# Kernel optimization log

Measured on AMD Instinct MI355X. Metric: run time of the kernel, lower is better.

The kernel has to match this reference:

```python
import jax, jax.numpy as jnp
from jax import lax
import numpy as np

B, T, H = 4096, 512, 32


def _rnn_layer(xs, h0, Wih, Whh, bih, bhh):
    # xs: [T, B, in], h0: [B, H]. torch RNN tanh: h_t = tanh(x W_ih^T + b_ih + h W_hh^T + b_hh)
    def step(h, x_t):
        h = jnp.tanh(x_t @ Wih.T + bih + h @ Whh.T + bhh)
        return h, h
    h_last, ys = lax.scan(step, h0, xs)
    return ys, h_last  # ys: [T, B, H]


def setup_inputs() -> dict:
    key = jax.random.key(0)
    ks = jax.random.split(key, 12)
    s = 0.1  # keep tanh out of saturation
    return {
        "x": jax.random.normal(ks[0], (B, T, 1), jnp.float32),
        "h_state": jnp.zeros((2, B, H), jnp.float32),
        "Wih0": jax.random.normal(ks[1], (H, 1), jnp.float32) * s,
        "Whh0": jax.random.normal(ks[2], (H, H), jnp.float32) * s,
        "bih0": jax.random.normal(ks[3], (H,), jnp.float32) * s,
        "bhh0": jax.random.normal(ks[4], (H,), jnp.float32) * s,
        "Wih1": jax.random.normal(ks[5], (H, H), jnp.float32) * s,
        "Whh1": jax.random.normal(ks[6], (H, H), jnp.float32) * s,
        "bih1": jax.random.normal(ks[7], (H,), jnp.float32) * s,
        "bhh1": jax.random.normal(ks[8], (H,), jnp.float32) * s,
        "Wfc": jax.random.normal(ks[9], (1, H), jnp.float32) * s,
        "bfc": jax.random.normal(ks[10], (1,), jnp.float32) * s,
    }


def reference(x, h_state, Wih0, Whh0, bih0, bhh0, Wih1, Whh1, bih1, bhh1, Wfc, bfc):
    xs = jnp.transpose(x, (1, 0, 2))  # time-major [T, B, 1]
    ys0, h0_last = _rnn_layer(xs, h_state[0], Wih0, Whh0, bih0, bhh0)
    ys1, h1_last = _rnn_layer(ys0, h_state[1], Wih1, Whh1, bih1, bhh1)
    last = ys1[-1]                      # [B, H] == r_out[:, -1, :]
    pred = (last @ Wfc.T + bfc)[:, 0]   # Linear(32,1) then squeeze(-1) -> [B]
    h_new = jnp.stack([h0_last, h1_last], axis=0)  # [2, B, H]
    return pred, h_new
```

## Files before the change

### kernel.cpp

```cpp
#include <hip/hip_runtime.h>
#include <hip/hip_bf16.h>

#define BB 4096
#define TT 512
#define HH 32

typedef __attribute__((ext_vector_type(8))) short short8;
typedef __attribute__((ext_vector_type(4))) float f32x4;

#define MFMA16 __builtin_amdgcn_mfma_f32_16x16x32_bf16
#define EXP2F  __builtin_amdgcn_exp2f

union frag_u { short8 s8; __hip_bfloat162 b2[4]; };

__global__ __launch_bounds__(64) void rnn2_mfma(
    const float* __restrict__ x,
    const float* __restrict__ hstate,
    const float* __restrict__ Wih0,
    const float* __restrict__ Whh0,
    const float* __restrict__ bih0,
    const float* __restrict__ bhh0,
    const float* __restrict__ Wih1,
    const float* __restrict__ Whh1,
    const float* __restrict__ bih1,
    const float* __restrict__ bhh1,
    const float* __restrict__ Wfc,
    const float* __restrict__ bfc,
    float* __restrict__ out)
{
    const int l = threadIdx.x;
    const int q = l >> 4;
    const int n = l & 15;
    const int b = blockIdx.x * 16 + n;

    const float SC = 2.8853900817779268f;

    const int r0 = 8 * (n >> 2) + (n & 3);
    short8 A0[2], A1i[2], A1h[2];
#pragma unroll
    for (int t = 0; t < 2; ++t) {
        const int row = r0 + 4 * t;
        const float* p0 = Whh0 + row * HH + q * 8;
        const float* p1 = Wih1 + row * HH + q * 8;
        const float* p2 = Whh1 + row * HH + q * 8;
        frag_u f0, f1, f2;
#pragma unroll
        for (int jj = 0; jj < 4; ++jj) {
            f0.b2[jj] = __float22bfloat162_rn(float2{SC * p0[2 * jj], SC * p0[2 * jj + 1]});
            f1.b2[jj] = __float22bfloat162_rn(float2{SC * p1[2 * jj], SC * p1[2 * jj + 1]});
            f2.b2[jj] = __float22bfloat162_rn(float2{SC * p2[2 * jj], SC * p2[2 * jj + 1]});
        }
        A0[t] = f0.s8; A1i[t] = f1.s8; A1h[t] = f2.s8;
    }

    float wxs[8], b0s[8], b1s[8], wfc8[8];
#pragma unroll
    for (int j = 0; j < 8; ++j) {
        const int hh = 8 * q + j;
        wxs[j]  = SC * Wih0[hh];
        b0s[j]  = SC * (bih0[hh] + bhh0[hh]);
        b1s[j]  = SC * (bih1[hh] + bhh1[hh]);
        wfc8[j] = Wfc[hh];
    }
    f32x4 c1t0, c1t1;
#pragma unroll
    for (int r = 0; r < 4; ++r) { c1t0[r] = b1s[r]; c1t1[r] = b1s[4 + r]; }

    frag_u h0f, h1f;
    {
        const float* p0 = hstate + b * HH + 8 * q;
        const float* p1 = hstate + BB * HH + b * HH + 8 * q;
#pragma unroll
        for (int jj = 0; jj < 4; ++jj) {
            h0f.b2[jj] = __float22bfloat162_rn(float2{p0[2 * jj], p0[2 * jj + 1]});
            h1f.b2[jj] = __float22bfloat162_rn(float2{p1[2 * jj], p1[2 * jj + 1]});
        }
    }
    short8 hb0 = h0f.s8, hb1 = h1f.s8;

    float hf0[8], hf1[8];

    const float4* xp = (const float4*)(x + (size_t)b * TT);
    float4 xv = xp[0];

    for (int t4 = 0; t4 < TT / 4; ++t4) {
        float4 xn = xp[(t4 < TT / 4 - 1) ? t4 + 1 : t4];
#pragma unroll
        for (int jj = 0; jj < 4; ++jj) {
            const float xt = (jj == 0) ? xv.x : (jj == 1) ? xv.y : (jj == 2) ? xv.z : xv.w;

            f32x4 db0 = MFMA16(A1h[0], hb1, c1t0, 0, 0, 0);
            f32x4 db1 = MFMA16(A1h[1], hb1, c1t1, 0, 0, 0);

            f32x4 c00, c01;
#pragma unroll
            for (int r = 0; r < 4; ++r) {
                c00[r] = fmaf(wxs[r], xt, b0s[r]);
                c01[r] = fmaf(wxs[4 + r], xt, b0s[4 + r]);
            }
            f32x4 d00 = MFMA16(A0[0], hb0, c00, 0, 0, 0);
            f32x4 d01 = MFMA16(A0[1], hb0, c01, 0, 0, 0);

            frag_u nh0;
#pragma unroll
            for (int r = 0; r < 4; ++r) {
                float e0 = EXP2F(d00[r]);
                float e1 = EXP2F(d01[r]);
                hf0[r]     = fmaf(-2.0f, __builtin_amdgcn_rcpf(e0 + 1.0f), 1.0f);
                hf0[4 + r] = fmaf(-2.0f, __builtin_amdgcn_rcpf(e1 + 1.0f), 1.0f);
            }
#pragma unroll
            for (int p2 = 0; p2 < 4; ++p2)
                nh0.b2[p2] = __float22bfloat162_rn(float2{hf0[2 * p2], hf0[2 * p2 + 1]});
            hb0 = nh0.s8;

            f32x4 d10 = MFMA16(A1i[0], hb0, db0, 0, 0, 0);
            f32x4 d11 = MFMA16(A1i[1], hb0, db1, 0, 0, 0);

            frag_u nh1;
#pragma unroll
            for (int r = 0; r < 4; ++r) {
                float e0 = EXP2F(d10[r]);
                float e1 = EXP2F(d11[r]);
                hf1[r]     = fmaf(-2.0f, __builtin_amdgcn_rcpf(e0 + 1.0f), 1.0f);
                hf1[4 + r] = fmaf(-2.0f, __builtin_amdgcn_rcpf(e1 + 1.0f), 1.0f);
            }
#pragma unroll
            for (int p2 = 0; p2 < 4; ++p2)
                nh1.b2[p2] = __float22bfloat162_rn(float2{hf1[2 * p2], hf1[2 * p2 + 1]});
            hb1 = nh1.s8;
        }
        xv = xn;
    }

    float p = 0.f;
#pragma unroll
    for (int j = 0; j < 8; ++j) p = fmaf(wfc8[j], hf1[j], p);
    p += __shfl_xor(p, 16);
    p += __shfl_xor(p, 32);
    if (q == 0) out[b] = p + bfc[0];

#pragma unroll
    for (int j = 0; j < 8; ++j) {
        out[BB + b * HH + 8 * q + j]           = hf0[j];
        out[BB + BB * HH + b * HH + 8 * q + j] = hf1[j];
    }
}

extern "C" void kernel_launch(void* const* d_in, const int* in_sizes, int n_in,
                              void* d_out, int out_size, void* d_ws, size_t ws_size,
                              hipStream_t stream) {
    const float* x      = (const float*)d_in[0];
    const float* hstate = (const float*)d_in[1];
    const float* Wih0   = (const float*)d_in[2];
    const float* Whh0   = (const float*)d_in[3];
    const float* bih0   = (const float*)d_in[4];
    const float* bhh0   = (const float*)d_in[5];
    const float* Wih1   = (const float*)d_in[6];
    const float* Whh1   = (const float*)d_in[7];
    const float* bih1   = (const float*)d_in[8];
    const float* bhh1   = (const float*)d_in[9];
    const float* Wfc    = (const float*)d_in[10];
    const float* bfc    = (const float*)d_in[11];
    float* out = (float*)d_out;

    dim3 grid(BB / 16);
    dim3 block(64);
    hipLaunchKernelGGL(rnn2_mfma, grid, block, 0, stream,
                       x, hstate, Wih0, Whh0, bih0, bhh0,
                       Wih1, Whh1, bih1, bhh1, Wfc, bfc, out);
}
```

Baseline: 223.7 us.

## Skew layer-1 and layer-0 recurrences so their MFMAs and tanh work interleave

Restructures the time loop so that layer 1 at step t and layer 0 at step t+1 run in the same iteration, with a prologue and epilogue. Each iteration issues the layer-1 input MFMAs and the next layer-0 MFMAs together, then interleaves both tanh chains. The aim is to break the serial dependency of the original order, where layer 1 waited on the freshly computed layer-0 state, and so hide MFMA and transcendental latency in this single-wave-per-block kernel. It adds code size and register pressure, and the indexing of x in the prologue and epilogue has to stay correct.

```diff
diff --git a/kernel.cpp b/kernel.cpp
--- a/kernel.cpp
+++ b/kernel.cpp
@@ -79,58 +79,103 @@
     short8 hb0 = h0f.s8, hb1 = h1f.s8;
 
     float hf0[8], hf1[8];
+    f32x4 dbp0, dbp1;
 
     const float4* xp = (const float4*)(x + (size_t)b * TT);
-    float4 xv = xp[0];
-
-    for (int t4 = 0; t4 < TT / 4; ++t4) {
-        float4 xn = xp[(t4 < TT / 4 - 1) ? t4 + 1 : t4];
-#pragma unroll
-        for (int jj = 0; jj < 4; ++jj) {
-            const float xt = (jj == 0) ? xv.x : (jj == 1) ? xv.y : (jj == 2) ? xv.z : xv.w;
-
-            f32x4 db0 = MFMA16(A1h[0], hb1, c1t0, 0, 0, 0);
-            f32x4 db1 = MFMA16(A1h[1], hb1, c1t1, 0, 0, 0);
-
-            f32x4 c00, c01;
-#pragma unroll
-            for (int r = 0; r < 4; ++r) {
-                c00[r] = fmaf(wxs[r], xt, b0s[r]);
-                c01[r] = fmaf(wxs[4 + r], xt, b0s[4 + r]);
-            }
-            f32x4 d00 = MFMA16(A0[0], hb0, c00, 0, 0, 0);
-            f32x4 d01 = MFMA16(A0[1], hb0, c01, 0, 0, 0);
-
-            frag_u nh0;
-#pragma unroll
-            for (int r = 0; r < 4; ++r) {
-                float e0 = EXP2F(d00[r]);
-                float e1 = EXP2F(d01[r]);
-                hf0[r]     = fmaf(-2.0f, __builtin_amdgcn_rcpf(e0 + 1.0f), 1.0f);
-                hf0[4 + r] = fmaf(-2.0f, __builtin_amdgcn_rcpf(e1 + 1.0f), 1.0f);
-            }
-#pragma unroll
-            for (int p2 = 0; p2 < 4; ++p2)
-                nh0.b2[p2] = __float22bfloat162_rn(float2{hf0[2 * p2], hf0[2 * p2 + 1]});
-            hb0 = nh0.s8;
-
-            f32x4 d10 = MFMA16(A1i[0], hb0, db0, 0, 0, 0);
-            f32x4 d11 = MFMA16(A1i[1], hb0, db1, 0, 0, 0);
-
-            frag_u nh1;
-#pragma unroll
-            for (int r = 0; r < 4; ++r) {
-                float e0 = EXP2F(d10[r]);
-                float e1 = EXP2F(d11[r]);
-                hf1[r]     = fmaf(-2.0f, __builtin_amdgcn_rcpf(e0 + 1.0f), 1.0f);
-                hf1[4 + r] = fmaf(-2.0f, __builtin_amdgcn_rcpf(e1 + 1.0f), 1.0f);
-            }
-#pragma unroll
-            for (int p2 = 0; p2 < 4; ++p2)
-                nh1.b2[p2] = __float22bfloat162_rn(float2{hf1[2 * p2], hf1[2 * p2 + 1]});
-            hb1 = nh1.s8;
-        }
-        xv = xn;
+    float4 xc = xp[0];
+
+    {
+        f32x4 c00, c01;
+#pragma unroll
+        for (int r = 0; r < 4; ++r) {
+            c00[r] = fmaf(wxs[r], xc.x, b0s[r]);
+            c01[r] = fmaf(wxs[4 + r], xc.x, b0s[4 + r]);
+        }
+        f32x4 d00 = MFMA16(A0[0], hb0, c00, 0, 0, 0);
+        f32x4 d01 = MFMA16(A0[1], hb0, c01, 0, 0, 0);
+        dbp0 = MFMA16(A1h[0], hb1, c1t0, 0, 0, 0);
+        dbp1 = MFMA16(A1h[1], hb1, c1t1, 0, 0, 0);
+        frag_u nh0;
+#pragma unroll
+        for (int r = 0; r < 4; ++r) {
+            float e0 = EXP2F(d00[r]);
+            float e1 = EXP2F(d01[r]);
+            hf0[r]     = fmaf(-2.0f, __builtin_amdgcn_rcpf(e0 + 1.0f), 1.0f);
+            hf0[4 + r] = fmaf(-2.0f, __builtin_amdgcn_rcpf(e1 + 1.0f), 1.0f);
+        }
+#pragma unroll
+        for (int p2 = 0; p2 < 4; ++p2)
+            nh0.b2[p2] = __float22bfloat162_rn(float2{hf0[2 * p2], hf0[2 * p2 + 1]});
+        hb0 = nh0.s8;
+    }
+
+#define STEP(XT)                                                              \
+    {                                                                         \
+            \
+        f32x4 d10 = MFMA16(A1i[0], hb0, dbp0, 0, 0, 0);                       \
+        f32x4 d11 = MFMA16(A1i[1], hb0, dbp1, 0, 0, 0);                       \
+                                                             \
+        f32x4 c00, c01;                                                       \
+        _Pragma("unroll")                                                     \
+        for (int r = 0; r < 4; ++r) {                                         \
+            c00[r] = fmaf(wxs[r], (XT), b0s[r]);                              \
+            c01[r] = fmaf(wxs[4 + r], (XT), b0s[4 + r]);                      \
+        }                                                                     \
+        f32x4 d00 = MFMA16(A0[0], hb0, c00, 0, 0, 0);                         \
+        f32x4 d01 = MFMA16(A0[1], hb0, c01, 0, 0, 0);                         \
+                           \
+        frag_u nh1;                                                           \
+        _Pragma("unroll")                                                     \
+        for (int r = 0; r < 4; ++r) {                                         \
+            float e0 = EXP2F(d10[r]);                                         \
+            float e1 = EXP2F(d11[r]);                                         \
+            hf1[r]     = fmaf(-2.0f, __builtin_amdgcn_rcpf(e0 + 1.0f), 1.0f); \
+            hf1[4 + r] = fmaf(-2.0f, __builtin_amdgcn_rcpf(e1 + 1.0f), 1.0f); \
+        }                                                                     \
+        _Pragma("unroll")                                                     \
+        for (int p2 = 0; p2 < 4; ++p2)                                        \
+            nh1.b2[p2] = __float22bfloat162_rn(float2{hf1[2 * p2], hf1[2 * p2 + 1]}); \
+        hb1 = nh1.s8;                                                         \
+                                       \
+        dbp0 = MFMA16(A1h[0], hb1, c1t0, 0, 0, 0);                            \
+        dbp1 = MFMA16(A1h[1], hb1, c1t1, 0, 0, 0);                            \
+                                \
+        frag_u nh0;                                                           \
+        _Pragma("unroll")                                                     \
+        for (int r = 0; r < 4; ++r) {                                         \
+            float e0 = EXP2F(d00[r]);                                         \
+            float e1 = EXP2F(d01[r]);                                         \
+            hf0[r]     = fmaf(-2.0f, __builtin_amdgcn_rcpf(e0 + 1.0f), 1.0f); \
+            hf0[4 + r] = fmaf(-2.0f, __builtin_amdgcn_rcpf(e1 + 1.0f), 1.0f); \
+        }                                                                     \
+        _Pragma("unroll")                                                     \
+        for (int p2 = 0; p2 < 4; ++p2)                                        \
+            nh0.b2[p2] = __float22bfloat162_rn(float2{hf0[2 * p2], hf0[2 * p2 + 1]}); \
+        hb0 = nh0.s8;                                                         \
+    }
+
+    for (int k = 0; k < TT / 4 - 1; ++k) {
+        float4 xn = xp[k + 1];
+        STEP(xc.y);
+        STEP(xc.z);
+        STEP(xc.w);
+        STEP(xn.x);
+        xc = xn;
+    }
+    STEP(xc.y);
+    STEP(xc.z);
+    STEP(xc.w);
+
+    {
+        f32x4 d10 = MFMA16(A1i[0], hb0, dbp0, 0, 0, 0);
+        f32x4 d11 = MFMA16(A1i[1], hb0, dbp1, 0, 0, 0);
+#pragma unroll
+        for (int r = 0; r < 4; ++r) {
+            float e0 = EXP2F(d10[r]);
+            float e1 = EXP2F(d11[r]);
+            hf1[r]     = fmaf(-2.0f, __builtin_amdgcn_rcpf(e0 + 1.0f), 1.0f);
+            hf1[4 + r] = fmaf(-2.0f, __builtin_amdgcn_rcpf(e1 + 1.0f), 1.0f);
+        }
     }
 
     float p = 0.f;
```

Measured after the change: 230.7 us. 3.1% more time.
